# Kernel tuning notes

Measured on AMD Instinct MI355X. Metric: run time of the kernel, lower is better.

Reference implementation:

```python
import jax, jax.numpy as jnp
import numpy as np

B, N, DIM, H, DH = 2, 2048, 256, 8, 32
DIM_INNER = H * DH  # 256


def setup_inputs() -> dict:
    key = jax.random.key(0)
    ks = jax.random.split(key, 8)
    s = DIM ** -0.5  # keep activations / logits in a sane range
    return {
        "x_real": jax.random.normal(ks[0], (B, N, DIM), jnp.float32),
        "x_imag": jax.random.normal(ks[1], (B, N, DIM), jnp.float32),
        "wq_r": jax.random.normal(ks[2], (DIM, DIM_INNER), jnp.float32) * s,
        "wq_i": jax.random.normal(ks[3], (DIM, DIM_INNER), jnp.float32) * s,
        "wkv_r": jax.random.normal(ks[4], (DIM, 2 * DIM_INNER), jnp.float32) * s,
        "wkv_i": jax.random.normal(ks[5], (DIM, 2 * DIM_INNER), jnp.float32) * s,
        "wo_r": jax.random.normal(ks[6], (DIM_INNER, DIM), jnp.float32) * s,
        "wo_i": jax.random.normal(ks[7], (DIM_INNER, DIM), jnp.float32) * s,
    }


def _clin(xr, xi, wr, wi):
    # complex linear: (xr + i xi) @ (wr + i wi)
    return xr @ wr - xi @ wi, xr @ wi + xi @ wr


def _split_heads(t):
    b, n, _ = t.shape
    return t.reshape(b, n, H, DH).transpose(0, 2, 1, 3)  # b h n d


def _merge_heads(t):
    b, h, n, d = t.shape
    return t.transpose(0, 2, 1, 3).reshape(b, n, h * d)


def reference(x_real, x_imag, wq_r, wq_i, wkv_r, wkv_i, wo_r, wo_i):
    # complex projections
    qr, qi = _clin(x_real, x_imag, wq_r, wq_i)
    kvr, kvi = _clin(x_real, x_imag, wkv_r, wkv_i)
    kr, vr = jnp.split(kvr, 2, axis=-1)
    ki, vi = jnp.split(kvi, 2, axis=-1)
    qr, qi, kr, ki, vr, vi = map(_split_heads, (qr, qi, kr, ki, vr, vi))

    # complex_attention_complete (sec 3.2 eq 3): 4 real SDPA replicas.
    # q repeat '(c r b)' -> blocks [qr, qr, qi, qi]; k repeat '(r c b)' -> [kr, ki, kr, ki]
    scale = DH ** -0.5
    Q = jnp.stack([qr, qr, qi, qi])        # [4, b, h, n, d]
    K = jnp.stack([kr, ki, kr, ki])
    sim = jnp.einsum('rbhid,rbhjd->rbhij', Q, K) * scale
    A = jax.nn.softmax(sim, axis=-1)       # [4, b, h, n, n]

    av = lambda a, v: jnp.einsum('bhij,bhjd->bhid', a, v)
    # sign-recombine trick: indices [0,3,5,6 | 1,2,4,7], sign [[1,-1,-1,-1],[1,1,1,-1]]
    o_r = av(A[0], vr) - av(A[1], vi) - av(A[2], vi) - av(A[3], vr)
    o_i = av(A[0], vi) + av(A[1], vr) + av(A[2], vr) - av(A[3], vi)

    mr, mi = _merge_heads(o_r), _merge_heads(o_i)
    out_r, out_i = _clin(mr, mi, wo_r, wo_i)
    # real view of the complex output: [b, n, dim, 2]
    return jnp.stack([out_r, out_i], axis=-1)
```

## Files before the change

### kernel.cpp

```cpp
#include <hip/hip_runtime.h>
#include <math.h>

namespace {
constexpr int kB = 2, kN = 2048, kDim = 256, kH = 8, kDH = 32;
constexpr int kBH = kB * kH;
constexpr long kPlane = (long)kBH * kN * kDH;
constexpr float kQScaleL2 = 0.25506852552f;
}

typedef unsigned short u16;
typedef short short8 __attribute__((ext_vector_type(8)));
typedef short short4v __attribute__((ext_vector_type(4)));
typedef float floatx16 __attribute__((ext_vector_type(16)));
#define MFMA_BF16(a, b, c) __builtin_amdgcn_mfma_f32_32x32x16_bf16(a, b, c, 0, 0, 0)

__device__ inline u16 bf16b(float x) {
    union { float f; unsigned u; } c; c.f = x;
    unsigned r = c.u + 0x7FFFu + ((c.u >> 16) & 1u);
    return (u16)(r >> 16);
}
__device__ inline unsigned pack2(float x, float y) {
    return (unsigned)bf16b(x) | ((unsigned)bf16b(y) << 16);
}
__device__ inline unsigned packtr(float lo, float hi) {
    return __builtin_amdgcn_perm(__float_as_uint(hi), __float_as_uint(lo), 0x07060302u);
}
__device__ inline short8 mk8(const float* e) {
    union { unsigned u[4]; short8 s; } c;
    c.u[0] = packtr(e[0], e[1]);
    c.u[1] = packtr(e[2], e[3]);
    c.u[2] = packtr(e[4], e[5]);
    c.u[3] = packtr(e[6], e[7]);
    return c.s;
}

__global__ __launch_bounds__(256, 2) void prep_w(
    const float* __restrict__ wq_r, const float* __restrict__ wq_i,
    const float* __restrict__ wkv_r, const float* __restrict__ wkv_i,
    const float* __restrict__ wo_r, const float* __restrict__ wo_i,
    u16* __restrict__ Wbig, u16* __restrict__ WoT)
{
    const long base = ((long)blockIdx.x * 256 + threadIdx.x) * 4;
    if (base < 786432) {
        const int c = (int)(base >> 9);
        const int k = (int)(base & 511);
        const int g = c >> 8, d = c & 255;
        const bool hi = k >= 256;
        const int k2 = hi ? k - 256 : k;
        const float* src;
        float sgn = 1.f;
        int col, stride;
        if (g < 2) {
            stride = 256; col = d;
            if (g == 0) { src = hi ? wq_i : wq_r; if (hi) sgn = -1.f; }
            else        { src = hi ? wq_r : wq_i; }
            sgn *= kQScaleL2;
        } else {
            stride = 512;
            col = (g >= 4) ? d + 256 : d;
            if ((g & 1) == 0) { src = hi ? wkv_i : wkv_r; if (hi) sgn = -1.f; }
            else              { src = hi ? wkv_r : wkv_i; }
        }
        short4v v;
        #pragma unroll
        for (int j = 0; j < 4; ++j)
            v[j] = (short)bf16b(src[(long)(k2 + j) * stride + col] * sgn);
        *(short4v*)(Wbig + base) = v;
    } else {
        const long o = base - 786432;
        const int c = (int)(o >> 9);
        const int k = (int)(o & 511);
        const bool hi = k >= 256;
        const int k2 = hi ? k - 256 : k;
        const float* src;
        float sgn = 1.f;
        int col;
        if (c < 256) { col = c;       src = hi ? wo_i : wo_r; if (hi) sgn = -1.f; }
        else         { col = c - 256; src = hi ? wo_r : wo_i; }
        short4v v;
        #pragma unroll
        for (int j = 0; j < 4; ++j)
            v[j] = (short)bf16b(src[(long)(k2 + j) * 256 + col] * sgn);
        *(short4v*)(WoT + o) = v;
    }
}

__global__ __launch_bounds__(256, 2) void gemm_proj(
    const float* __restrict__ xr_g, const float* __restrict__ xi_g,
    const u16* __restrict__ BT,
    u16* __restrict__ qr, u16* __restrict__ qi, u16* __restrict__ kr,
    u16* __restrict__ ki, u16* __restrict__ vrT, u16* __restrict__ viT)
{
    __shared__ __align__(16) u16 sA[128 * 32];
    __shared__ __align__(16) u16 sB[128 * 32];
    const int tid = threadIdx.x;
    const int lane = tid & 63, l31 = lane & 31, lh = lane >> 5;
    const int w = tid >> 6, wrow = w & 1, wcol = w >> 1;
    const int srow = tid >> 2, sseg = tid & 3;
    const int n0 = blockIdx.x * 128, m0 = blockIdx.y * 128;

    floatx16 a00 = {0}, a01 = {0}, a10 = {0}, a11 = {0};

    for (int kt = 0; kt < 512; kt += 32) {
        __syncthreads();
        const float* xbase = (kt < 256) ? xr_g : xi_g;
        const int kc = (kt & 255) + sseg * 8;
        #pragma unroll
        for (int i = 0; i < 2; ++i) {
            const int r = srow + i * 64;
            {
                const float* src = xbase + (long)(m0 + r) * 256 + kc;
                const float4 f0 = *(const float4*)(src);
                const float4 f1 = *(const float4*)(src + 4);
                short8 v;
                v[0] = (short)bf16b(f0.x); v[1] = (short)bf16b(f0.y);
                v[2] = (short)bf16b(f0.z); v[3] = (short)bf16b(f0.w);
                v[4] = (short)bf16b(f1.x); v[5] = (short)bf16b(f1.y);
                v[6] = (short)bf16b(f1.z); v[7] = (short)bf16b(f1.w);
                *(short8*)(sA + r * 32 + sseg * 8) = v;
            }
            *(short8*)(sB + r * 32 + sseg * 8) =
                *(const short8*)(BT + (long)(n0 + r) * 512 + kt + sseg * 8);
        }
        __syncthreads();
        #pragma unroll
        for (int s = 0; s < 2; ++s) {
            const int ko = s * 16 + lh * 8;
            const short8 fa0 = *(const short8*)(sA + (wrow * 64 + l31) * 32 + ko);
            const short8 fa1 = *(const short8*)(sA + (wrow * 64 + 32 + l31) * 32 + ko);
            const short8 fb0 = *(const short8*)(sB + (wcol * 64 + l31) * 32 + ko);
            const short8 fb1 = *(const short8*)(sB + (wcol * 64 + 32 + l31) * 32 + ko);
            a00 = MFMA_BF16(fa0, fb0, a00);
            a01 = MFMA_BF16(fa0, fb1, a01);
            a10 = MFMA_BF16(fa1, fb0, a10);
            a11 = MFMA_BF16(fa1, fb1, a11);
        }
    }

    floatx16 accs[2][2] = {{a00, a01}, {a10, a11}};
    #pragma unroll
    for (int rt = 0; rt < 2; ++rt) {
        #pragma unroll
        for (int ct = 0; ct < 2; ++ct) {
            const int colb = n0 + wcol * 64 + ct * 32;
            const int g = colb >> 8;
            const int h = (colb & 255) >> 5;
            if (g < 4) {
                u16* pl = (g == 0) ? qr : (g == 1) ? qi : (g == 2) ? kr : ki;
                #pragma unroll
                for (int reg = 0; reg < 16; ++reg) {
                    const int row = m0 + wrow * 64 + rt * 32 + (reg & 3) + 8 * (reg >> 2) + 4 * lh;
                    const int b = row >> 11, nn = row & 2047;
                    pl[(((long)(b * 8 + h)) * 2048 + nn) * 32 + l31] = bf16b(accs[rt][ct][reg]);
                }
            } else {
                u16* pl = (g == 4) ? vrT : viT;
                #pragma unroll
                for (int reg = 0; reg < 16; ++reg) {
                    const int row = m0 + wrow * 64 + rt * 32 + (reg & 3) + 8 * (reg >> 2) + 4 * lh;
                    const int b = row >> 11, nn = row & 2047;
                    const int np = (nn & ~12) | ((nn & 4) << 1) | ((nn & 8) >> 1);
                    pl[(((long)(b * 8 + h)) * 32 + l31) * 2048 + np] = bf16b(accs[rt][ct][reg]);
                }
            }
        }
    }
}

__global__ __launch_bounds__(256, 4) void attn_kernel(
    const u16* __restrict__ qr_g, const u16* __restrict__ qi_g,
    const u16* __restrict__ kr_g, const u16* __restrict__ ki_g,
    const u16* __restrict__ vrT_g, const u16* __restrict__ viT_g,
    u16* __restrict__ xo)
{
    __shared__ __align__(16) u16 smem[2][2][64 * 40];

    const int tid = threadIdx.x;
    const int lane = tid & 63, l31 = lane & 31, lh = lane >> 5;
    const int w = tid >> 6, ktype = w & 1, qtype = w >> 1;
    const int bh = blockIdx.x;
    const int i0 = blockIdx.y * 32;
    const long base = (long)bh * kN * kDH;

    const u16* qg = (qtype ? qi_g : qr_g) + base;
    short8 qB0, qB1;
    {
        const u16* qp = qg + (long)(i0 + l31) * kDH;
        qB0 = *(const short8*)(qp + lh * 8);
        qB1 = *(const short8*)(qp + 16 + lh * 8);
    }

    const int srow = tid & 63;
    const int sseg = tid >> 6;
    const u16* kptr = ((srow < 32) ? kr_g : ki_g) + base
                    + (long)(srow & 31) * kDH + sseg * 8;
    const u16* vptr = ((srow < 32) ? vrT_g : viT_g)
                    + ((long)bh * 32 + (srow & 31)) * kN + sseg * 8;

    short8 kreg = *(const short8*)kptr;
    short8 vreg = *(const short8*)vptr;

    floatx16 Ur = {0}, Ui = {0};
    float La = 0.f;

    for (int t = 0; t < 64; ++t) {
        u16* bK = smem[0][t & 1];
        u16* bV = smem[1][t & 1];
        *(short8*)(bK + srow * 40 + sseg * 8) = kreg;
        *(short8*)(bV + srow * 40 + sseg * 8) = vreg;
        __syncthreads();
        if (t < 63) {
            kreg = *(const short8*)(kptr + (long)(t + 1) * 1024);
            vreg = *(const short8*)(vptr + (t + 1) * 32);
        }

        const short8 ka0 = *(const short8*)(bK + (ktype * 32 + l31) * 40 + lh * 8);
        const short8 ka1 = *(const short8*)(bK + (ktype * 32 + l31) * 40 + 16 + lh * 8);
        floatx16 S = {0};
        S = MFMA_BF16(ka0, qB0, S);
        S = MFMA_BF16(ka1, qB1, S);

        float e[16];
        #pragma unroll
        for (int r = 0; r < 16; ++r) {
            e[r] = __builtin_amdgcn_exp2f(S[r]);
            La += e[r];
        }
        const short8 Fa = mk8(&e[0]);
        const short8 Fb = mk8(&e[8]);

        const short8 va0 = *(const short8*)(bV + l31 * 40 + lh * 8);
        const short8 va1 = *(const short8*)(bV + l31 * 40 + 16 + lh * 8);
        const short8 vb0 = *(const short8*)(bV + (32 + l31) * 40 + lh * 8);
        const short8 vb1 = *(const short8*)(bV + (32 + l31) * 40 + 16 + lh * 8);

        Ur = MFMA_BF16(va0, Fa, Ur);
        Ur = MFMA_BF16(va1, Fb, Ur);
        Ui = MFMA_BF16(vb0, Fa, Ui);
        Ui = MFMA_BF16(vb1, Fb, Ui);
    }

    La += __shfl_xor(La, 32);
    const float iL = 1.f / La;

    float cr[16], ci[16];
    #pragma unroll
    for (int r = 0; r < 16; ++r) {
        if (w == 0)      { cr[r] =  Ur[r] * iL; ci[r] =  Ui[r] * iL; }
        else if (w == 3) { cr[r] = -Ur[r] * iL; ci[r] = -Ui[r] * iL; }
        else             { cr[r] = -Ui[r] * iL; ci[r] =  Ur[r] * iL; }
    }

    __syncthreads();
    float* sC = (float*)smem;
    if (qtype == 1) {
        float* dst = sC + ktype * 2048;
        #pragma unroll
        for (int r = 0; r < 16; ++r) {
            dst[r * 64 + lane] = cr[r];
            dst[1024 + r * 64 + lane] = ci[r];
        }
    }
    __syncthreads();
    if (qtype == 0) {
        float* s = sC + ktype * 2048;
        #pragma unroll
        for (int r = 0; r < 16; ++r) {
            cr[r] += s[r * 64 + lane];
            ci[r] += s[1024 + r * 64 + lane];
        }
        if (ktype == 1) {
            #pragma unroll
            for (int r = 0; r < 16; ++r) {
                s[r * 64 + lane] = cr[r];
                s[1024 + r * 64 + lane] = ci[r];
            }
        }
    }
    __syncthreads();
    if (w == 0) {
        const float* s = sC + 2048;
        #pragma unroll
        for (int r = 0; r < 16; ++r) {
            cr[r] += s[r * 64 + lane];
            ci[r] += s[1024 + r * 64 + lane];
        }
        const int b = bh >> 3, h = bh & 7;
        u16* xrow = xo + ((long)(b * 2048 + i0 + l31)) * 512 + h * 32;
        #pragma unroll
        for (int g = 0; g < 4; ++g) {
            const int d0 = 8 * g + 4 * lh;
            union { unsigned u[2]; uint2 v; } pr, pi;
            pr.u[0] = pack2(cr[4 * g + 0], cr[4 * g + 1]);
            pr.u[1] = pack2(cr[4 * g + 2], cr[4 * g + 3]);
            pi.u[0] = pack2(ci[4 * g + 0], ci[4 * g + 1]);
            pi.u[1] = pack2(ci[4 * g + 2], ci[4 * g + 3]);
            *(uint2*)(xrow + d0) = pr.v;
            *(uint2*)(xrow + 256 + d0) = pi.v;
        }
    }
}

__global__ __launch_bounds__(256, 2) void gemm_oproj(
    const u16* __restrict__ Xo, const u16* __restrict__ BT, float* __restrict__ out)
{
    __shared__ __align__(16) u16 sA[128 * 32];
    __shared__ __align__(16) u16 sB[128 * 32];
    const int tid = threadIdx.x;
    const int lane = tid & 63, l31 = lane & 31, lh = lane >> 5;
    const int w = tid >> 6, wrow = w & 1, wcol = w >> 1;
    const int srow = tid >> 2, sseg = tid & 3;
    const int n0 = blockIdx.x * 128, m0 = blockIdx.y * 128;

    floatx16 a00 = {0}, a01 = {0}, a10 = {0}, a11 = {0};

    for (int kt = 0; kt < 512; kt += 32) {
        __syncthreads();
        #pragma unroll
        for (int i = 0; i < 2; ++i) {
            const int r = srow + i * 64;
            *(short8*)(sA + r * 32 + sseg * 8) =
                *(const short8*)(Xo + (long)(m0 + r) * 512 + kt + sseg * 8);
            *(short8*)(sB + r * 32 + sseg * 8) =
                *(const short8*)(BT + (long)(n0 + r) * 512 + kt + sseg * 8);
        }
        __syncthreads();
        #pragma unroll
        for (int s = 0; s < 2; ++s) {
            const int ko = s * 16 + lh * 8;
            const short8 fa0 = *(const short8*)(sA + (wrow * 64 + l31) * 32 + ko);
            const short8 fa1 = *(const short8*)(sA + (wrow * 64 + 32 + l31) * 32 + ko);
            const short8 fb0 = *(const short8*)(sB + (wcol * 64 + l31) * 32 + ko);
            const short8 fb1 = *(const short8*)(sB + (wcol * 64 + 32 + l31) * 32 + ko);
            a00 = MFMA_BF16(fa0, fb0, a00);
            a01 = MFMA_BF16(fa0, fb1, a01);
            a10 = MFMA_BF16(fa1, fb0, a10);
            a11 = MFMA_BF16(fa1, fb1, a11);
        }
    }

    floatx16 accs[2][2] = {{a00, a01}, {a10, a11}};
    #pragma unroll
    for (int rt = 0; rt < 2; ++rt) {
        #pragma unroll
        for (int ct = 0; ct < 2; ++ct) {
            const int colb = n0 + wcol * 64 + ct * 32;
            #pragma unroll
            for (int reg = 0; reg < 16; ++reg) {
                const int row = m0 + wrow * 64 + rt * 32 + (reg & 3) + 8 * (reg >> 2) + 4 * lh;
                const int col = colb + l31;
                const float val = accs[rt][ct][reg];
                if (colb < 256) out[(long)row * 512 + col * 2] = val;
                else            out[(long)row * 512 + (col - 256) * 2 + 1] = val;
            }
        }
    }
}

extern "C" void kernel_launch(void* const* d_in, const int* in_sizes, int n_in,
                              void* d_out, int out_size, void* d_ws, size_t ws_size,
                              hipStream_t stream) {
    const float* xr    = (const float*)d_in[0];
    const float* xi    = (const float*)d_in[1];
    const float* wq_r  = (const float*)d_in[2];
    const float* wq_i  = (const float*)d_in[3];
    const float* wkv_r = (const float*)d_in[4];
    const float* wkv_i = (const float*)d_in[5];
    const float* wo_r  = (const float*)d_in[6];
    const float* wo_i  = (const float*)d_in[7];
    float* out = (float*)d_out;

    u16* ws16 = (u16*)d_ws;
    u16* qr   = ws16 + 0 * kPlane;
    u16* qi   = ws16 + 1 * kPlane;
    u16* kr   = ws16 + 2 * kPlane;
    u16* ki   = ws16 + 3 * kPlane;
    u16* vrT  = ws16 + 4 * kPlane;
    u16* viT  = ws16 + 5 * kPlane;
    u16* xo   = ws16 + 6 * kPlane;
    u16* Wbig = ws16 + 8 * kPlane;
    u16* WoT  = Wbig + 786432;

    prep_w<<<1024, 256, 0, stream>>>(wq_r, wq_i, wkv_r, wkv_i, wo_r, wo_i, Wbig, WoT);
    gemm_proj<<<dim3(12, 32), 256, 0, stream>>>(xr, xi, Wbig, qr, qi, kr, ki, vrT, viT);
    attn_kernel<<<dim3(kBH, kN / 32), 256, 0, stream>>>(qr, qi, kr, ki, vrT, viT, xo);
    gemm_oproj<<<dim3(4, 32), 256, 0, stream>>>(xo, WoT, out);
}
```

Baseline: 178.2 us.

## Load K fragments directly from global and compute row sums with MFMA

The attention loop stops staging K tiles through shared memory. Each wave now loads its K MFMA fragments straight from global memory into registers, prefetched one step ahead. The softmax denominator, previously 16 scalar adds plus a cross-lane shuffle, is now accumulated by two extra MFMAs against a ones vector. Exponentials are computed inside the bf16 packing helper. This trades fewer LDS writes, barriers and VALU adds for more MFMA work and uncoalesced direct global loads, and the denominator is now summed from bf16-rounded exponentials.

```diff
diff --git a/kernel.cpp b/kernel.cpp
--- a/kernel.cpp
+++ b/kernel.cpp
@@ -25,12 +25,12 @@
 __device__ inline unsigned packtr(float lo, float hi) {
     return __builtin_amdgcn_perm(__float_as_uint(hi), __float_as_uint(lo), 0x07060302u);
 }
-__device__ inline short8 mk8(const float* e) {
+__device__ inline short8 mk8exp(const floatx16& S, int b) {
     union { unsigned u[4]; short8 s; } c;
-    c.u[0] = packtr(e[0], e[1]);
-    c.u[1] = packtr(e[2], e[3]);
-    c.u[2] = packtr(e[4], e[5]);
-    c.u[3] = packtr(e[6], e[7]);
+    #pragma unroll
+    for (int j = 0; j < 4; ++j)
+        c.u[j] = packtr(__builtin_amdgcn_exp2f(S[b + 2 * j]),
+                        __builtin_amdgcn_exp2f(S[b + 2 * j + 1]));
     return c.s;
 }
 
@@ -173,7 +173,7 @@
     const u16* __restrict__ vrT_g, const u16* __restrict__ viT_g,
     u16* __restrict__ xo)
 {
-    __shared__ __align__(16) u16 smem[2][2][64 * 40];
+    __shared__ __align__(16) u16 smem[8192];
 
     const int tid = threadIdx.x;
     const int lane = tid & 63, l31 = lane & 31, lh = lane >> 5;
@@ -192,56 +192,54 @@
 
     const int srow = tid & 63;
     const int sseg = tid >> 6;
-    const u16* kptr = ((srow < 32) ? kr_g : ki_g) + base
-                    + (long)(srow & 31) * kDH + sseg * 8;
     const u16* vptr = ((srow < 32) ? vrT_g : viT_g)
                     + ((long)bh * 32 + (srow & 31)) * kN + sseg * 8;
-
-    short8 kreg = *(const short8*)kptr;
     short8 vreg = *(const short8*)vptr;
 
-    floatx16 Ur = {0}, Ui = {0};
-    float La = 0.f;
+    const u16* kAp = (ktype ? ki_g : kr_g) + base + (long)l31 * kDH + lh * 8;
+    short8 ka0 = *(const short8*)(kAp);
+    short8 ka1 = *(const short8*)(kAp + 16);
+
+    const short8 ones8 = {(short)0x3F80, (short)0x3F80, (short)0x3F80, (short)0x3F80,
+                          (short)0x3F80, (short)0x3F80, (short)0x3F80, (short)0x3F80};
+
+    floatx16 Ur = {0}, Ui = {0}, Lacc = {0};
 
     for (int t = 0; t < 64; ++t) {
-        u16* bK = smem[0][t & 1];
-        u16* bV = smem[1][t & 1];
-        *(short8*)(bK + srow * 40 + sseg * 8) = kreg;
+        u16* bV = smem + (t & 1) * 2560;
         *(short8*)(bV + srow * 40 + sseg * 8) = vreg;
         __syncthreads();
         if (t < 63) {
-            kreg = *(const short8*)(kptr + (long)(t + 1) * 1024);
             vreg = *(const short8*)(vptr + (t + 1) * 32);
         }
-
-        const short8 ka0 = *(const short8*)(bK + (ktype * 32 + l31) * 40 + lh * 8);
-        const short8 ka1 = *(const short8*)(bK + (ktype * 32 + l31) * 40 + 16 + lh * 8);
-        floatx16 S = {0};
-        S = MFMA_BF16(ka0, qB0, S);
-        S = MFMA_BF16(ka1, qB1, S);
-
-        float e[16];
-        #pragma unroll
-        for (int r = 0; r < 16; ++r) {
-            e[r] = __builtin_amdgcn_exp2f(S[r]);
-            La += e[r];
-        }
-        const short8 Fa = mk8(&e[0]);
-        const short8 Fb = mk8(&e[8]);
 
         const short8 va0 = *(const short8*)(bV + l31 * 40 + lh * 8);
         const short8 va1 = *(const short8*)(bV + l31 * 40 + 16 + lh * 8);
         const short8 vb0 = *(const short8*)(bV + (32 + l31) * 40 + lh * 8);
         const short8 vb1 = *(const short8*)(bV + (32 + l31) * 40 + 16 + lh * 8);
 
+        floatx16 S = {0};
+        S = MFMA_BF16(ka0, qB0, S);
+        S = MFMA_BF16(ka1, qB1, S);
+        if (t < 63) {
+            const long ko = (long)(t + 1) * 1024;
+            ka0 = *(const short8*)(kAp + ko);
+            ka1 = *(const short8*)(kAp + ko + 16);
+        }
+
+        const short8 Fa = mk8exp(S, 0);
+        const short8 Fb = mk8exp(S, 8);
+
+        Lacc = MFMA_BF16(ones8, Fa, Lacc);
+        Lacc = MFMA_BF16(ones8, Fb, Lacc);
+
         Ur = MFMA_BF16(va0, Fa, Ur);
         Ur = MFMA_BF16(va1, Fb, Ur);
         Ui = MFMA_BF16(vb0, Fa, Ui);
         Ui = MFMA_BF16(vb1, Fb, Ui);
     }
 
-    La += __shfl_xor(La, 32);
-    const float iL = 1.f / La;
+    const float iL = 1.f / Lacc[0];
 
     float cr[16], ci[16];
     #pragma unroll
```

New measurement: 186.4 us. 1.05x slower.

## Load K directly to registers and software-pipeline QK^T with the PV MFMAs

Applied to the files above, without the earlier changes.

K fragments are now read straight from global memory into registers, two tiles ahead, instead of being staged through shared memory. The next tile's QK^T MFMAs are issued before the current tile's PV MFMAs, so exp2 and the softmax work can overlap with matrix-core work. The row-sum accumulator is split into four partial sums, PV MFMAs run under raised wave priority, and blocks get staggered s_sleep delays at start. This trades more register pressure and redundant global K loads (each wave pair loads its own K) for less LDS traffic and better instruction overlap.

```diff
diff --git a/kernel.cpp b/kernel.cpp
--- a/kernel.cpp
+++ b/kernel.cpp
@@ -53,7 +53,7 @@
         if (g < 2) {
             stride = 256; col = d;
             if (g == 0) { src = hi ? wq_i : wq_r; if (hi) sgn = -1.f; }
-            else        { src = hi ? wq_r : wq_i; }
+        else        { src = hi ? wq_r : wq_i; }
             sgn *= kQScaleL2;
         } else {
             stride = 512;
@@ -173,7 +173,7 @@
     const u16* __restrict__ vrT_g, const u16* __restrict__ viT_g,
     u16* __restrict__ xo)
 {
-    __shared__ __align__(16) u16 smem[2][2][64 * 40];
+    __shared__ __align__(16) u16 smem[8192];
 
     const int tid = threadIdx.x;
     const int lane = tid & 63, l31 = lane & 31, lh = lane >> 5;
@@ -182,6 +182,16 @@
     const int i0 = blockIdx.y * 32;
     const long base = (long)bh * kN * kDH;
 
+    {
+        const int rnd = ((blockIdx.x + 16 * blockIdx.y) >> 8) & 3;
+        switch (rnd) {
+            case 1: __builtin_amdgcn_s_sleep(2); break;
+            case 2: __builtin_amdgcn_s_sleep(4); break;
+            case 3: __builtin_amdgcn_s_sleep(6); break;
+            default: break;
+        }
+    }
+
     const u16* qg = (qtype ? qi_g : qr_g) + base;
     short8 qB0, qB1;
     {
@@ -192,54 +202,70 @@
 
     const int srow = tid & 63;
     const int sseg = tid >> 6;
-    const u16* kptr = ((srow < 32) ? kr_g : ki_g) + base
-                    + (long)(srow & 31) * kDH + sseg * 8;
     const u16* vptr = ((srow < 32) ? vrT_g : viT_g)
                     + ((long)bh * 32 + (srow & 31)) * kN + sseg * 8;
-
-    short8 kreg = *(const short8*)kptr;
     short8 vreg = *(const short8*)vptr;
 
+    const u16* kAp = (ktype ? ki_g : kr_g) + base + (long)l31 * kDH + lh * 8;
+    short8 ka0 = *(const short8*)(kAp);
+    short8 ka1 = *(const short8*)(kAp + 16);
+    short8 kn0 = *(const short8*)(kAp + 1024);
+    short8 kn1 = *(const short8*)(kAp + 1024 + 16);
+
     floatx16 Ur = {0}, Ui = {0};
-    float La = 0.f;
+    float La0 = 0.f, La1 = 0.f, La2 = 0.f, La3 = 0.f;
+
+    floatx16 S = {0};
+    S = MFMA_BF16(ka0, qB0, S);
+    S = MFMA_BF16(ka1, qB1, S);
+    ka0 = kn0; ka1 = kn1;
 
     for (int t = 0; t < 64; ++t) {
-        u16* bK = smem[0][t & 1];
-        u16* bV = smem[1][t & 1];
-        *(short8*)(bK + srow * 40 + sseg * 8) = kreg;
+        u16* bV = smem + (t & 1) * 2560;
         *(short8*)(bV + srow * 40 + sseg * 8) = vreg;
         __syncthreads();
         if (t < 63) {
-            kreg = *(const short8*)(kptr + (long)(t + 1) * 1024);
             vreg = *(const short8*)(vptr + (t + 1) * 32);
         }
-
-        const short8 ka0 = *(const short8*)(bK + (ktype * 32 + l31) * 40 + lh * 8);
-        const short8 ka1 = *(const short8*)(bK + (ktype * 32 + l31) * 40 + 16 + lh * 8);
-        floatx16 S = {0};
-        S = MFMA_BF16(ka0, qB0, S);
-        S = MFMA_BF16(ka1, qB1, S);
-
-        float e[16];
-        #pragma unroll
-        for (int r = 0; r < 16; ++r) {
-            e[r] = __builtin_amdgcn_exp2f(S[r]);
-            La += e[r];
-        }
-        const short8 Fa = mk8(&e[0]);
-        const short8 Fb = mk8(&e[8]);
+        if (t < 62) {
+            kn0 = *(const short8*)(kAp + (long)(t + 2) * 1024);
+            kn1 = *(const short8*)(kAp + (long)(t + 2) * 1024 + 16);
+        }
 
         const short8 va0 = *(const short8*)(bV + l31 * 40 + lh * 8);
         const short8 va1 = *(const short8*)(bV + l31 * 40 + 16 + lh * 8);
         const short8 vb0 = *(const short8*)(bV + (32 + l31) * 40 + lh * 8);
         const short8 vb1 = *(const short8*)(bV + (32 + l31) * 40 + 16 + lh * 8);
 
+        float e[16];
+        #pragma unroll
+        for (int r = 0; r < 16; ++r) e[r] = __builtin_amdgcn_exp2f(S[r]);
+        #pragma unroll
+        for (int r = 0; r < 16; r += 4) {
+            La0 += e[r + 0]; La1 += e[r + 1];
+            La2 += e[r + 2]; La3 += e[r + 3];
+        }
+        const short8 Fa = mk8(&e[0]);
+        const short8 Fb = mk8(&e[8]);
+
+        floatx16 Sn = {0};
+        if (t < 63) {
+            Sn = MFMA_BF16(ka0, qB0, Sn);
+            Sn = MFMA_BF16(ka1, qB1, Sn);
+        }
+
+        __builtin_amdgcn_s_setprio(1);
         Ur = MFMA_BF16(va0, Fa, Ur);
         Ur = MFMA_BF16(va1, Fb, Ur);
         Ui = MFMA_BF16(vb0, Fa, Ui);
         Ui = MFMA_BF16(vb1, Fb, Ui);
-    }
-
+        __builtin_amdgcn_s_setprio(0);
+
+        S = Sn;
+        ka0 = kn0; ka1 = kn1;
+    }
+
+    float La = (La0 + La1) + (La2 + La3);
     La += __shfl_xor(La, 32);
     const float iL = 1.f / La;
 
```

Measured after the change: 184.6 us. 3.6% more time.

## Process two key tiles per barrier in attention loop with split accumulators

Applied to the files above, without the earlier changes.

The attention main loop now stages two 32-key K/V tiles per iteration into a doubled shared-memory buffer, halving the number of __syncthreads barriers and global-load rounds. Score MFMAs for both tiles are issued up front, the softmax row sum is split across four independent accumulators to break the add dependency chain, and the PV MFMAs are wrapped in s_setprio hints. Doubling LDS and lowering launch bounds from 4 to 3 blocks per CU gives the compiler more registers but reduces occupancy.

```diff
diff --git a/kernel.cpp b/kernel.cpp
--- a/kernel.cpp
+++ b/kernel.cpp
@@ -167,13 +167,13 @@
     }
 }
 
-__global__ __launch_bounds__(256, 4) void attn_kernel(
+__global__ __launch_bounds__(256, 3) void attn_kernel(
     const u16* __restrict__ qr_g, const u16* __restrict__ qi_g,
     const u16* __restrict__ kr_g, const u16* __restrict__ ki_g,
     const u16* __restrict__ vrT_g, const u16* __restrict__ viT_g,
     u16* __restrict__ xo)
 {
-    __shared__ __align__(16) u16 smem[2][2][64 * 40];
+    __shared__ __align__(16) u16 smem[2][4][64 * 40];
 
     const int tid = threadIdx.x;
     const int lane = tid & 63, l31 = lane & 31, lh = lane >> 5;
@@ -197,49 +197,90 @@
     const u16* vptr = ((srow < 32) ? vrT_g : viT_g)
                     + ((long)bh * 32 + (srow & 31)) * kN + sseg * 8;
 
-    short8 kreg = *(const short8*)kptr;
-    short8 vreg = *(const short8*)vptr;
+    short8 krA = *(const short8*)(kptr);
+    short8 krB = *(const short8*)(kptr + 1024);
+    short8 vrA = *(const short8*)(vptr);
+    short8 vrB = *(const short8*)(vptr + 32);
 
     floatx16 Ur = {0}, Ui = {0};
-    float La = 0.f;
-
-    for (int t = 0; t < 64; ++t) {
-        u16* bK = smem[0][t & 1];
-        u16* bV = smem[1][t & 1];
-        *(short8*)(bK + srow * 40 + sseg * 8) = kreg;
-        *(short8*)(bV + srow * 40 + sseg * 8) = vreg;
+    float La0 = 0.f, La1 = 0.f, La2 = 0.f, La3 = 0.f;
+
+    for (int t = 0; t < 32; ++t) {
+        u16* buf = (u16*)smem[t & 1];
+        *(short8*)(buf + 0 * 2560 + srow * 40 + sseg * 8) = krA;
+        *(short8*)(buf + 1 * 2560 + srow * 40 + sseg * 8) = krB;
+        *(short8*)(buf + 2 * 2560 + srow * 40 + sseg * 8) = vrA;
+        *(short8*)(buf + 3 * 2560 + srow * 40 + sseg * 8) = vrB;
         __syncthreads();
-        if (t < 63) {
-            kreg = *(const short8*)(kptr + (long)(t + 1) * 1024);
-            vreg = *(const short8*)(vptr + (t + 1) * 32);
-        }
-
-        const short8 ka0 = *(const short8*)(bK + (ktype * 32 + l31) * 40 + lh * 8);
-        const short8 ka1 = *(const short8*)(bK + (ktype * 32 + l31) * 40 + 16 + lh * 8);
-        floatx16 S = {0};
-        S = MFMA_BF16(ka0, qB0, S);
-        S = MFMA_BF16(ka1, qB1, S);
-
-        float e[16];
-        #pragma unroll
-        for (int r = 0; r < 16; ++r) {
-            e[r] = __builtin_amdgcn_exp2f(S[r]);
-            La += e[r];
-        }
-        const short8 Fa = mk8(&e[0]);
-        const short8 Fb = mk8(&e[8]);
-
-        const short8 va0 = *(const short8*)(bV + l31 * 40 + lh * 8);
-        const short8 va1 = *(const short8*)(bV + l31 * 40 + 16 + lh * 8);
-        const short8 vb0 = *(const short8*)(bV + (32 + l31) * 40 + lh * 8);
-        const short8 vb1 = *(const short8*)(bV + (32 + l31) * 40 + 16 + lh * 8);
-
-        Ur = MFMA_BF16(va0, Fa, Ur);
-        Ur = MFMA_BF16(va1, Fb, Ur);
-        Ui = MFMA_BF16(vb0, Fa, Ui);
-        Ui = MFMA_BF16(vb1, Fb, Ui);
-    }
-
+        if (t < 31) {
+            krA = *(const short8*)(kptr + (long)(t + 1) * 2048);
+            krB = *(const short8*)(kptr + (long)(t + 1) * 2048 + 1024);
+            vrA = *(const short8*)(vptr + (t + 1) * 64);
+            vrB = *(const short8*)(vptr + (t + 1) * 64 + 32);
+        }
+        const u16* bKa = buf;
+        const u16* bKb = buf + 2560;
+        const u16* bVa = buf + 5120;
+        const u16* bVb = buf + 7680;
+
+        const short8 kfA0 = *(const short8*)(bKa + (ktype * 32 + l31) * 40 + lh * 8);
+        const short8 kfA1 = *(const short8*)(bKa + (ktype * 32 + l31) * 40 + 16 + lh * 8);
+        const short8 kfB0 = *(const short8*)(bKb + (ktype * 32 + l31) * 40 + lh * 8);
+        const short8 kfB1 = *(const short8*)(bKb + (ktype * 32 + l31) * 40 + 16 + lh * 8);
+        floatx16 Sa = {0}, Sb = {0};
+        Sa = MFMA_BF16(kfA0, qB0, Sa);
+        Sa = MFMA_BF16(kfA1, qB1, Sa);
+        Sb = MFMA_BF16(kfB0, qB0, Sb);
+        Sb = MFMA_BF16(kfB1, qB1, Sb);
+
+        float ea[16];
+        #pragma unroll
+        for (int r = 0; r < 16; ++r) ea[r] = __builtin_amdgcn_exp2f(Sa[r]);
+        #pragma unroll
+        for (int r = 0; r < 16; r += 4) {
+            La0 += ea[r + 0]; La1 += ea[r + 1];
+            La2 += ea[r + 2]; La3 += ea[r + 3];
+        }
+        const short8 FaA = mk8(&ea[0]);
+        const short8 FbA = mk8(&ea[8]);
+        {
+            const short8 va0 = *(const short8*)(bVa + l31 * 40 + lh * 8);
+            const short8 va1 = *(const short8*)(bVa + l31 * 40 + 16 + lh * 8);
+            const short8 vb0 = *(const short8*)(bVa + (32 + l31) * 40 + lh * 8);
+            const short8 vb1 = *(const short8*)(bVa + (32 + l31) * 40 + 16 + lh * 8);
+            __builtin_amdgcn_s_setprio(1);
+            Ur = MFMA_BF16(va0, FaA, Ur);
+            Ur = MFMA_BF16(va1, FbA, Ur);
+            Ui = MFMA_BF16(vb0, FaA, Ui);
+            Ui = MFMA_BF16(vb1, FbA, Ui);
+            __builtin_amdgcn_s_setprio(0);
+        }
+
+        float eb[16];
+        #pragma unroll
+        for (int r = 0; r < 16; ++r) eb[r] = __builtin_amdgcn_exp2f(Sb[r]);
+        #pragma unroll
+        for (int r = 0; r < 16; r += 4) {
+            La0 += eb[r + 0]; La1 += eb[r + 1];
+            La2 += eb[r + 2]; La3 += eb[r + 3];
+        }
+        const short8 FaB = mk8(&eb[0]);
+        const short8 FbB = mk8(&eb[8]);
+        {
+            const short8 va0 = *(const short8*)(bVb + l31 * 40 + lh * 8);
+            const short8 va1 = *(const short8*)(bVb + l31 * 40 + 16 + lh * 8);
+            const short8 vb0 = *(const short8*)(bVb + (32 + l31) * 40 + lh * 8);
+            const short8 vb1 = *(const short8*)(bVb + (32 + l31) * 40 + 16 + lh * 8);
+            __builtin_amdgcn_s_setprio(1);
+            Ur = MFMA_BF16(va0, FaB, Ur);
+            Ur = MFMA_BF16(va1, FbB, Ur);
+            Ui = MFMA_BF16(vb0, FaB, Ui);
+            Ui = MFMA_BF16(vb1, FbB, Ui);
+            __builtin_amdgcn_s_setprio(0);
+        }
+    }
+
+    float La = (La0 + La1) + (La2 + La3);
     La += __shfl_xor(La, 32);
     const float iL = 1.f / La;
 
```

Result: slower. 184.9 us (+3.8%).
